# Kernel optimization log

Hardware: AMD Instinct MI355X
Metric: run time of the kernel (lower is better)

Reference implementation:

```python
import jax, jax.numpy as jnp
import numpy as np

# ---- constants from init_kwargs (mode='local', channel='G') ----
MEAN = 127.5
STD = 50.0
BINS = np.array([-2.4, -1.6, -0.8, 0.0, 0.8, 1.6, 2.4])
NB = len(BINS) + 1            # 8 quantization levels
DIST = [1, 2, 3]
THETA = [0.0, np.pi / 4, np.pi / 2, 3 * np.pi / 4]
MASK = 17
STRIDE = 4
BIN_EDGES = 0.5 + BINS / 6.0
# skimage greycomatrix offsets: (round(sin(t)*d), round(cos(t)*d)), ordered d-major
OFFSETS = [(int(np.round(np.sin(t) * d)), int(np.round(np.cos(t) * d)))
           for d in DIST for t in THETA]


def setup_inputs() -> dict:
    key = jax.random.key(0)
    x = jax.random.uniform(key, (8, 3, 256, 256), dtype=jnp.float32) * 255.0
    return {"x": x}


def _features(x):
    img = x[:, 1, :, :]                       # channel 'G'
    img = jnp.where(img < 10.0, 0.0, img)     # imgs[imgs < 10] = 0
    B, H, W = img.shape
    N = (H - MASK) // STRIDE + 1              # 60 windows per axis

    # sliding windows -> (B, N, N, MASK, MASK)
    r = (jnp.arange(N) * STRIDE)[:, None] + jnp.arange(MASK)[None, :]
    win = img[:, r[:, None, :, None], r[None, :, None, :]]
    Nw = B * N * N
    flat = win.reshape(Nw, MASK * MASK)

    # ---- stat over nonzero pixels (numpy population std) ----
    mask = flat != 0.0
    n_safe = jnp.maximum(mask.sum(-1), 1).astype(flat.dtype)
    mean = jnp.where(mask, flat, 0.0).sum(-1) / n_safe
    std = jnp.sqrt((jnp.where(mask, flat - mean[:, None], 0.0) ** 2).sum(-1) / n_safe)
    mx = jnp.where(mask, flat, -jnp.inf).max(-1)
    mn = jnp.where(mask, flat, jnp.inf).min(-1)
    stat = jnp.stack([mean, std, (mx - mean) / (std + 1e-9), (mean - mn) / (std + 1e-9)], -1)

    # ---- quantize ----
    q = jnp.digitize(((flat - MEAN) / STD + 3.0) / 6.0, jnp.asarray(BIN_EDGES, flat.dtype))

    # ---- histogram (density over ALL pixels, drop first & last bin) ----
    onehot = (q[..., None] == jnp.arange(NB)).astype(flat.dtype)
    hist_feat = onehot.sum(1)[:, 1:NB - 1] / flat.shape[1]   # (Nw, len(BINS)-1)

    # ---- GLCM per (dist, theta) offset, symmetric + normed ----
    qm = q.reshape(Nw, MASK, MASK)
    rows = jnp.arange(Nw)[:, None]
    glcms = []
    for dr, dc in OFFSETS:
        if dc >= 0:
            i = qm[:, :MASK - dr, :MASK - dc]
            j = qm[:, dr:, dc:]
        else:
            i = qm[:, :MASK - dr, -dc:]
            j = qm[:, dr:, :MASK + dc]
        pair = (i * NB + j).reshape(Nw, -1)
        cnt = jnp.zeros((Nw, NB * NB), flat.dtype).at[rows, pair].add(1.0)
        P = cnt.reshape(Nw, NB, NB)
        P = P + P.transpose(0, 2, 1)                               # symmetric
        P = P / jnp.maximum(P.sum((1, 2), keepdims=True), 1e-12)   # normed
        glcms.append(P)
    G = jnp.stack(glcms, 1)          # (Nw, 12, NB, NB)
    g = G[:, :, 1:, 1:]              # crop level 0 (zeros)
    L = NB - 1

    # greycoprops renormalizes the (cropped) GLCM internally
    Pn = g / jnp.maximum(g.sum((2, 3), keepdims=True), 1e-12)
    I = jnp.arange(L, dtype=flat.dtype)
    diff2 = (I[:, None] - I[None, :]) ** 2
    contrast = (Pn * diff2).sum((2, 3))
    homog = (Pn / (1.0 + diff2)).sum((2, 3))
    energy = jnp.sqrt((Pn ** 2).sum((2, 3)))
    Pi = Pn.sum(3)
    Pj = Pn.sum(2)
    mui = (Pi * I).sum(-1)
    muj = (Pj * I).sum(-1)
    sdi = jnp.sqrt((Pi * (I - mui[..., None]) ** 2).sum(-1))
    sdj = jnp.sqrt((Pj * (I - muj[..., None]) ** 2).sum(-1))
    cov = (Pn * (I[:, None] - mui[..., None, None]) * (I[None, :] - muj[..., None, None])).sum((2, 3))
    corr = jnp.where(sdi * sdj < 1e-15, 1.0, cov / jnp.maximum(sdi * sdj, 1e-15))
    entropy = -(g * jnp.log2(g + 1e-8)).sum((2, 3))   # on cropped, non-renormed g

    glcm_feat = jnp.concatenate([contrast, homog, energy, corr, entropy], -1)  # (Nw, 60)
    feats = jnp.concatenate([stat, hist_feat, glcm_feat], -1)                  # (Nw, 70)

    # windows with max == 0 yield all-zero feature vectors
    feats = jnp.where((flat.max(-1) == 0.0)[:, None], 0.0, feats)

    Fdim = feats.shape[-1]
    feats = feats.reshape(B, N, N, Fdim)
    total = feats.sum((1, 2))
    nz = (feats != 0).sum((1, 2)).astype(flat.dtype)
    return total / (nz + 1e-9)            # (B, 70)


def reference(x):
    return _features(x)
```

## Files before the change

kernel.cpp:

```cpp
#include <hip/hip_runtime.h>
#include <cmath>

#define NPIX   289
#define NU     10
#define NF     70
#define NWX    60
#define IMG_W  256
#define IMG_HW 65536
#define NWIN   28800
#define ACC    560
#define WPB    4
#define NBLK   (NWIN / WPB)

__device__ __constant__ int c_s2u[12] = {0,1,2,3,4,1,5,3,6,7,8,9};

constexpr int DRu[NU] = {0, 1, 1, 1, 0, 2, 0, 2, 3, 2};
constexpr int DCu[NU] = {1, 1, 0,-1, 2, 0, 3, 2, 0,-2};
constexpr int JOFF[NU] = {1, 18, 17, 16, 2, 34, 3, 36, 51, 32};
constexpr float INV2N[NU] = {1.f/544.f, 1.f/512.f, 1.f/544.f, 1.f/512.f, 1.f/510.f,
                             1.f/510.f, 1.f/476.f, 1.f/450.f, 1.f/476.f, 1.f/450.f};

struct VTab { unsigned w[NU][10]; };
constexpr VTab make_vtab() {
    VTab t{};
    for (int o = 0; o < NU; ++o)
        for (int idx = 0; idx < NPIX; ++idx) {
            int r = idx / 17, c = idx % 17, cc = c + DCu[o];
            if (r + DRu[o] <= 16 && cc >= 0 && cc <= 16)
                t.w[o][idx >> 5] |= 1u << (idx & 31);
        }
    return t;
}
constexpr VTab c_vt = make_vtab();

__device__ __forceinline__ float wsum(float v){ for(int o=32;o;o>>=1) v += __shfl_xor(v,o,64); return v; }
__device__ __forceinline__ float wmax(float v){ for(int o=32;o;o>>=1) v = fmaxf(v,__shfl_xor(v,o,64)); return v; }
__device__ __forceinline__ float wmin(float v){ for(int o=32;o;o>>=1) v = fminf(v,__shfl_xor(v,o,64)); return v; }

__global__ __launch_bounds__(256) void feat_kernel(const float* __restrict__ x,
                                                   float* __restrict__ ptot,
                                                   float* __restrict__ pnz,
                                                   int setmask) {
    __shared__ float s_g[WPB][NU * 49];
    __shared__ float s_uf[WPB][5][NU];
    __shared__ float s_s10[WPB][10];

    const int lane = threadIdx.x & 63;
    const int wid  = threadIdx.x >> 6;
    const int widx = blockIdx.x * WPB + wid;
    const int b    = widx / 3600;
    const int rem  = widx - b * 3600;
    const int wy   = rem / NWX;
    const int wx   = rem - wy * NWX;
    const float* img = x + (size_t)(b * 3 + 1) * IMG_HW + (wy * 4) * IMG_W + wx * 4;

    float* gl  = s_g[wid];
    float (*uf)[NU] = s_uf[wid];
    float* s10 = s_s10[wid];

    const int l49 = (lane < 49) ? lane : 48;
    const int ba  = l49 / 7 + 1;
    const int bb  = l49 - (ba - 1) * 7 + 1;
    const unsigned long long xm0a = (ba & 1) ? 0ull : ~0ull;
    const unsigned long long xm1a = (ba & 2) ? 0ull : ~0ull;
    const unsigned long long xm2a = (ba & 4) ? 0ull : ~0ull;
    const unsigned long long xm0b = (bb & 1) ? 0ull : ~0ull;
    const unsigned long long xm1b = (bb & 2) ? 0ull : ~0ull;
    const unsigned long long xm2b = (bb & 4) ? 0ull : ~0ull;

    float lsum = 0.f, lss = 0.f, lmax = -1e30f, lmin = 1e30f;
    int n = 0, c1 = 0, c2 = 0, c3 = 0, c4 = 0, c5 = 0, c6 = 0;
    unsigned ma32[10], mb32[12];
#pragma unroll
    for (int k = 0; k < 5; ++k) {
        const int t = lane + k * 64;
        float val = 0.f;
        if (t < NPIX) {
            const int r = t / 17;
            float p = img[r * (IMG_W - 17) + t];
            val = (p < 10.f) ? 0.f : p;
        }
        float qf = fminf(fmaxf(floorf(fmaf(val, 0.025f, -1.1875f)) + 1.f, 0.f), 6.f);
        int qq = (val != 0.f) ? ((int)qf + 1) : 0;
        lsum += val;
        float d = (val != 0.f) ? (val - 127.5f) : 0.f;
        lss = fmaf(d, d, lss);
        lmax = fmaxf(lmax, val);
        lmin = fminf(lmin, (val != 0.f) ? val : 1e30f);
        unsigned long long p0 = __ballot(qq & 1);
        unsigned long long p1 = __ballot(qq & 2);
        unsigned long long p2 = __ballot(qq & 4);
        n  += __popcll(p0 | p1 | p2);
        c1 += __popcll(p0 & ~p1 & ~p2);
        c2 += __popcll(~p0 & p1 & ~p2);
        c3 += __popcll(p0 & p1 & ~p2);
        c4 += __popcll(~p0 & ~p1 & p2);
        c5 += __popcll(p0 & ~p1 & p2);
        c6 += __popcll(~p0 & p1 & p2);
        unsigned long long mA = (p0 ^ xm0a) & (p1 ^ xm1a) & (p2 ^ xm2a);
        unsigned long long mB = (p0 ^ xm0b) & (p1 ^ xm1b) & (p2 ^ xm2b);
        ma32[2*k]   = (unsigned)mA;  ma32[2*k+1] = (unsigned)(mA >> 32);
        mb32[2*k]   = (unsigned)mB;  mb32[2*k+1] = (unsigned)(mB >> 32);
    }
    mb32[10] = 0u; mb32[11] = 0u;

    if (n == 0) return;

    const float fn   = (float)n;
    const float sum  = wsum(lsum);
    const float ss   = wsum(lss);
    const float mx   = wmax(lmax);
    const float mn   = wmin(lmin);
    const float mean = sum / fn;
    const float mc   = mean - 127.5f;
    const float var  = fmaxf(ss / fn - mc * mc, 0.f);
    const float stdv = sqrtf(var);

    if (lane == 0) {
        s10[0] = mean;
        s10[1] = stdv;
        s10[2] = (mx - mean) / (stdv + 1e-9f);
        s10[3] = (mean - mn) / (stdv + 1e-9f);
        s10[4] = (float)c1 * (1.f / 289.f);
        s10[5] = (float)c2 * (1.f / 289.f);
        s10[6] = (float)c3 * (1.f / 289.f);
        s10[7] = (float)c4 * (1.f / 289.f);
        s10[8] = (float)c5 * (1.f / 289.f);
        s10[9] = (float)c6 * (1.f / 289.f);
    }

    int cnta[NU];
#pragma unroll
    for (int o = 0; o < NU; ++o) {
        const int wq = JOFF[o] >> 5;
        const int r  = JOFF[o] & 31;
        int acc = 0;
#pragma unroll
        for (int w = 0; w < 10; ++w) {
            unsigned mav = ma32[w] & c_vt.w[o][w];
            unsigned sh  = __builtin_amdgcn_alignbit(mb32[w + wq + 1], mb32[w + wq], r);
            acc += __popc(mav & sh);
        }
        cnta[o] = acc;
    }

    const int partner = (bb - 1) * 7 + (ba - 1);
#pragma unroll
    for (int o = 0; o < NU; ++o) {
        int pc = __shfl(cnta[o], partner, 64);
        float g = (float)(cnta[o] + pc) * INV2N[o];
        if (lane < 49) gl[o * 49 + l49] = g;
    }

    const int fo  = lane & 15;
    const int sub = lane >> 4;
    float gsum=0.f, entU=0.f, conU=0.f, homU=0.f, g2=0.f, siU=0.f, siiU=0.f, sijU=0.f;
    if (fo < NU) {
        for (int idx = sub; idx < 49; idx += 4) {
            float g = gl[fo * 49 + idx];
            int fi = (idx * 37) >> 8;
            int fj = idx - fi * 7;
            float d  = (float)(fi - fj);
            float d2 = d * d;
            float ffi = (float)fi, ffj = (float)fj;
            gsum += g;
            entU += g * __log2f(g + 1e-8f);
            conU += g * d2;
            homU += g * __builtin_amdgcn_rcpf(1.f + d2);
            g2   += g * g;
            siU  += g * ffi;
            siiU += g * ffi * ffi;
            sijU += g * ffi * ffj;
        }
    }
#pragma unroll
    for (int s = 16; s <= 32; s <<= 1) {
        gsum += __shfl_xor(gsum, s, 64);  entU += __shfl_xor(entU, s, 64);
        conU += __shfl_xor(conU, s, 64);  homU += __shfl_xor(homU, s, 64);
        g2   += __shfl_xor(g2,   s, 64);  siU  += __shfl_xor(siU,  s, 64);
        siiU += __shfl_xor(siiU, s, 64);  sijU += __shfl_xor(sijU, s, 64);
    }
    if (fo < NU && sub == 0) {
        const float invg = 1.f / fmaxf(gsum, 1e-12f);
        const float si  = siU  * invg;
        const float sii = siiU * invg;
        const float sij = sijU * invg;
        const float varg = fmaxf(sii - si * si, 0.f);
        const float cov  = sij - si * si;
        uf[0][fo] = conU * invg;
        uf[1][fo] = homU * invg;
        uf[2][fo] = sqrtf(g2) * invg;
        uf[3][fo] = (varg < 1e-15f) ? 1.f : cov / fmaxf(varg, 1e-15f);
        uf[4][fo] = -entU;
    }

    const int setbase = (widx & setmask) * ACC;
    const int obase   = b * NF;
    for (int t = lane; t < NF; t += 64) {
        float f;
        if (t < 10) {
            f = s10[t];
        } else {
            int u    = t - 10;
            int grp  = u / 12;
            int slot = u - grp * 12;
            f = uf[grp][c_s2u[slot]];
        }
        if (f != 0.f) {
            atomicAdd(&ptot[setbase + obase + t], f);
            atomicAdd(&pnz[setbase + obase + t], 1.f);
        }
    }
}

__global__ void reduce_kernel(const float* __restrict__ ptot,
                              const float* __restrict__ pnz,
                              float* __restrict__ out, int nset) {
    int t = blockIdx.x * blockDim.x + threadIdx.x;
    if (t >= ACC) return;
    float s = 0.f, nz = 0.f;
    for (int k = 0; k < nset; ++k) {
        s  += ptot[(size_t)k * ACC + t];
        nz += pnz[(size_t)k * ACC + t];
    }
    out[t] = s / (nz + 1e-9f);
}

extern "C" void kernel_launch(void* const* d_in, const int* in_sizes, int n_in,
                              void* d_out, int out_size, void* d_ws, size_t ws_size,
                              hipStream_t stream) {
    (void)in_sizes; (void)n_in; (void)out_size;
    const float* x = (const float*)d_in[0];
    float* out = (float*)d_out;

    const size_t per_set = (size_t)2 * ACC * sizeof(float);
    int maxs = (ws_size >= per_set) ? (int)(ws_size / per_set) : 1;
    int nset = 1;
    while ((nset * 2) <= maxs && nset < 64) nset <<= 1;

    float* ptot = (float*)d_ws;
    float* pnz  = ptot + (size_t)nset * ACC;

    hipMemsetAsync(d_ws, 0, (size_t)nset * per_set, stream);
    feat_kernel<<<dim3(NBLK), dim3(256), 0, stream>>>(x, ptot, pnz, nset - 1);
    reduce_kernel<<<dim3((ACC + 255) / 256), dim3(256), 0, stream>>>(ptot, pnz, out, nset);
}
```

Baseline: 122.2 us.

## Exploit GLCM symmetry, precompute column masks, simplify quantization, add occupancy bound

Stores only the 28 upper-triangle GLCM entries and reduces them with weights from a constant feature table, so the shared-memory reduction does 7 iterations per lane instead of 13. The per-offset validity mask is replaced by column masks applied once to the shifted bitplane and shared between offsets with the same column shift, and row-only offsets skip masking entirely with 9 words. Quantization becomes a single fmaf-and-truncate. The launch bound also requests 4 blocks per CU. The risks are subtle correctness issues at the mask and quantization edges, and extra register pressure.

Measured after the change: 123.7 us. About the same (+1.2%).

```diff
diff --git a/kernel.cpp b/kernel.cpp
--- a/kernel.cpp
+++ b/kernel.cpp
@@ -20,28 +20,62 @@
 constexpr float INV2N[NU] = {1.f/544.f, 1.f/512.f, 1.f/544.f, 1.f/512.f, 1.f/510.f,
                              1.f/510.f, 1.f/476.f, 1.f/450.f, 1.f/476.f, 1.f/450.f};
 
-struct VTab { unsigned w[NU][10]; };
-constexpr VTab make_vtab() {
-    VTab t{};
-    for (int o = 0; o < NU; ++o)
-        for (int idx = 0; idx < NPIX; ++idx) {
-            int r = idx / 17, c = idx % 17, cc = c + DCu[o];
-            if (r + DRu[o] <= 16 && cc >= 0 && cc <= 16)
-                t.w[o][idx >> 5] |= 1u << (idx & 31);
+struct CMs { unsigned m[10]; };
+constexpr CMs mkcm(int dc) {
+    CMs c{};
+    for (int t = 0; t < NPIX; ++t) {
+        int col = t % 17;
+        bool ok = (dc > 0) ? (col >= dc) : (col <= 16 + dc);
+        if (ok) c.m[t >> 5] |= 1u << (t & 31);
+    }
+    return c;
+}
+constexpr CMs CMp1 = mkcm(1), CMp2 = mkcm(2), CMp3 = mkcm(3);
+constexpr CMs CMn1 = mkcm(-1), CMn2 = mkcm(-2);
+
+struct alignas(32) FtE { float w, d2, inv, si, sii, sij, q0, q1; };
+struct FtTab { FtE e[28]; };
+constexpr FtTab mkft() {
+    FtTab t{};
+    int n = 0;
+    for (int a = 1; a <= 7; ++a)
+        for (int b = a; b <= 7; ++b) {
+            int i = a - 1, j = b - 1;
+            float w  = (a == b) ? 1.f : 2.f;
+            float d2 = (float)((i - j) * (i - j));
+            t.e[n] = FtE{w, d2, 1.f / (1.f + d2),
+                         0.5f * (float)(i + j),
+                         0.5f * (float)(i * i + j * j),
+                         (float)(i * j), 0.f, 0.f};
+            ++n;
         }
     return t;
 }
-constexpr VTab c_vt = make_vtab();
+__device__ __constant__ FtTab c_ft = mkft();
+
+template<int O>
+__device__ __forceinline__ int gcnt(const unsigned* M, const unsigned* ma) {
+    constexpr int wq = JOFF[O] >> 5;
+    constexpr int rr = JOFF[O] & 31;
+    int acc = 0;
+#pragma unroll
+    for (int w = 0; w < 9; ++w) {
+        unsigned sh = (rr == 0) ? M[w + wq]
+                    : __builtin_amdgcn_alignbit(M[w + wq + 1], M[w + wq], rr);
+        acc += __popc(ma[w] & sh);
+    }
+    return acc;
+}
 
 __device__ __forceinline__ float wsum(float v){ for(int o=32;o;o>>=1) v += __shfl_xor(v,o,64); return v; }
 __device__ __forceinline__ float wmax(float v){ for(int o=32;o;o>>=1) v = fmaxf(v,__shfl_xor(v,o,64)); return v; }
 __device__ __forceinline__ float wmin(float v){ for(int o=32;o;o>>=1) v = fminf(v,__shfl_xor(v,o,64)); return v; }
 
-__global__ __launch_bounds__(256) void feat_kernel(const float* __restrict__ x,
-                                                   float* __restrict__ ptot,
-                                                   float* __restrict__ pnz,
-                                                   int setmask) {
-    __shared__ float s_g[WPB][NU * 49];
+__global__ __launch_bounds__(256, 4) void feat_kernel(const float* __restrict__ x,
+                                                      float* __restrict__ ptot,
+                                                      float* __restrict__ pnz,
+                                                      int setmask) {
+    __shared__ float s_g[WPB][NU * 28];
     __shared__ float s_uf[WPB][5][NU];
     __shared__ float s_s10[WPB][10];
 
@@ -80,8 +114,7 @@
             float p = img[r * (IMG_W - 17) + t];
             val = (p < 10.f) ? 0.f : p;
         }
-        float qf = fminf(fmaxf(floorf(fmaf(val, 0.025f, -1.1875f)) + 1.f, 0.f), 6.f);
-        int qq = (val != 0.f) ? ((int)qf + 1) : 0;
+        int qq = min((int)fmaf(val, 0.025f, 0.8125f), 7);
         lsum += val;
         float d = (val != 0.f) ? (val - 127.5f) : 0.f;
         lss = fmaf(d, d, lss);
@@ -130,47 +163,60 @@
     }
 
     int cnta[NU];
-#pragma unroll
-    for (int o = 0; o < NU; ++o) {
-        const int wq = JOFF[o] >> 5;
-        const int r  = JOFF[o] & 31;
-        int acc = 0;
-#pragma unroll
-        for (int w = 0; w < 10; ++w) {
-            unsigned mav = ma32[w] & c_vt.w[o][w];
-            unsigned sh  = __builtin_amdgcn_alignbit(mb32[w + wq + 1], mb32[w + wq], r);
-            acc += __popc(mav & sh);
-        }
-        cnta[o] = acc;
+    {
+        unsigned mv[12]; mv[10] = 0u; mv[11] = 0u;
+        cnta[2] = gcnt<2>(mb32, ma32);
+        cnta[5] = gcnt<5>(mb32, ma32);
+        cnta[8] = gcnt<8>(mb32, ma32);
+#pragma unroll
+        for (int w = 0; w < 10; ++w) mv[w] = mb32[w] & CMp1.m[w];
+        cnta[0] = gcnt<0>(mv, ma32);
+        cnta[1] = gcnt<1>(mv, ma32);
+#pragma unroll
+        for (int w = 0; w < 10; ++w) mv[w] = mb32[w] & CMp2.m[w];
+        cnta[4] = gcnt<4>(mv, ma32);
+        cnta[7] = gcnt<7>(mv, ma32);
+#pragma unroll
+        for (int w = 0; w < 10; ++w) mv[w] = mb32[w] & CMp3.m[w];
+        cnta[6] = gcnt<6>(mv, ma32);
+#pragma unroll
+        for (int w = 0; w < 10; ++w) mv[w] = mb32[w] & CMn1.m[w];
+        cnta[3] = gcnt<3>(mv, ma32);
+#pragma unroll
+        for (int w = 0; w < 10; ++w) mv[w] = mb32[w] & CMn2.m[w];
+        cnta[9] = gcnt<9>(mv, ma32);
     }
 
     const int partner = (bb - 1) * 7 + (ba - 1);
+    const int amin  = min(ba, bb);
+    const int idx28 = 8 * (amin - 1) - ((amin * (amin - 1)) >> 1) + (max(ba, bb) - amin);
+    const bool wr   = (lane < 49) && (ba <= bb);
 #pragma unroll
     for (int o = 0; o < NU; ++o) {
         int pc = __shfl(cnta[o], partner, 64);
         float g = (float)(cnta[o] + pc) * INV2N[o];
-        if (lane < 49) gl[o * 49 + l49] = g;
+        if (wr) gl[o * 28 + idx28] = g;
     }
 
     const int fo  = lane & 15;
     const int sub = lane >> 4;
     float gsum=0.f, entU=0.f, conU=0.f, homU=0.f, g2=0.f, siU=0.f, siiU=0.f, sijU=0.f;
     if (fo < NU) {
-        for (int idx = sub; idx < 49; idx += 4) {
-            float g = gl[fo * 49 + idx];
-            int fi = (idx * 37) >> 8;
-            int fj = idx - fi * 7;
-            float d  = (float)(fi - fj);
-            float d2 = d * d;
-            float ffi = (float)fi, ffj = (float)fj;
-            gsum += g;
-            entU += g * __log2f(g + 1e-8f);
-            conU += g * d2;
-            homU += g * __builtin_amdgcn_rcpf(1.f + d2);
-            g2   += g * g;
-            siU  += g * ffi;
-            siiU += g * ffi * ffi;
-            sijU += g * ffi * ffj;
+#pragma unroll
+        for (int i = 0; i < 7; ++i) {
+            const int e = sub + 4 * i;
+            FtE c = c_ft.e[e];
+            float g  = gl[fo * 28 + e];
+            float gw = g * c.w;
+            float l  = __log2f(g + 1e-8f);
+            gsum += gw;
+            entU  = fmaf(gw, l,      entU);
+            conU  = fmaf(gw, c.d2,   conU);
+            homU  = fmaf(gw, c.inv,  homU);
+            g2    = fmaf(gw, g,      g2);
+            siU   = fmaf(gw, c.si,   siU);
+            siiU  = fmaf(gw, c.sii,  siiU);
+            sijU  = fmaf(gw, c.sij,  sijU);
         }
     }
 #pragma unroll
```
